# Performance work log

Measured on AMD Instinct MI355X. Metric: run time of the kernel, lower is better.

Reference implementation:

```python
import jax, jax.numpy as jnp
import numpy as np

NUM_AGENTS = 4
ACTOR_DIM = 128
OBS_DIM = 64
ACTION_SIZE = 16
BATCH = 65536


def _linear_params(key, din, dout):
    kw, kb = jax.random.split(key)
    bound = 1.0 / np.sqrt(din)
    W = jax.random.uniform(kw, (din, dout), jnp.float32, -bound, bound)
    b = jax.random.uniform(kb, (dout,), jnp.float32, -bound, bound)
    return W, b


def setup_inputs() -> dict:
    key = jax.random.key(0)
    ks = jax.random.split(key, 8)
    O = jax.random.normal(ks[0], (BATCH, NUM_AGENTS, OBS_DIM), jnp.float32)
    enc_w, enc_b = _linear_params(ks[1], OBS_DIM, ACTOR_DIM)
    fc1_w, fc1_b = _linear_params(ks[2], ACTOR_DIM, ACTOR_DIM)
    fc2_w, fc2_b = _linear_params(ks[3], ACTOR_DIM, ACTOR_DIM)
    fc3_w, fc3_b = _linear_params(ks[4], ACTOR_DIM, ACTOR_DIM)
    cl4_w, cl4_b = _linear_params(ks[5], 2 * ACTOR_DIM, ACTOR_DIM)
    dec_w, dec_b = _linear_params(ks[6], NUM_AGENTS * ACTOR_DIM, ACTION_SIZE)
    return {
        "O": O,
        "enc_w": enc_w, "enc_b": enc_b,
        "fc1_w": fc1_w, "fc1_b": fc1_b,
        "fc2_w": fc2_w, "fc2_b": fc2_b,
        "fc3_w": fc3_w, "fc3_b": fc3_b,
        "cl4_w": cl4_w, "cl4_b": cl4_b,
        "dec_w": dec_w, "dec_b": dec_b,
    }


def reference(O, enc_w, enc_b, fc1_w, fc1_b, fc2_w, fc2_b, fc3_w, fc3_b,
              cl4_w, cl4_b, dec_w, dec_b):
    # Encoding: sigmoid(Linear(obs)) -> [B, A, D]
    H0 = jax.nn.sigmoid(O @ enc_w + enc_b)
    H1 = jax.nn.relu(H0 @ fc1_w + fc1_b)
    H2 = jax.nn.relu(H1 @ fc2_w + fc2_b)
    H3 = jax.nn.relu(H2 @ fc3_w + fc3_b)
    # get_commvar: masked mean over OTHER agents, but torch divides by
    # num_agents (self slot is zeroed then included in the mean).
    # Equivalent fused form: C[b,i] = (sum_j H[b,j] - H[b,i]) / num_agents
    C = (jnp.sum(H3, axis=1, keepdims=True) - H3) / NUM_AGENTS
    H_cat = jnp.concatenate([H3, C], axis=-1)          # [B, A, 2D]
    H4 = H_cat @ cl4_w + cl4_b                          # [B, A, D] (no activation)
    H = H4.reshape(-1, NUM_AGENTS * ACTOR_DIM)          # [B, A*D]
    logits = H @ dec_w + dec_b                          # [B, action_size]
    return jax.nn.softmax(logits, axis=-1)
```

## Files before the change

kernel.cpp:

```cpp
#include <hip/hip_runtime.h>
#include <stdint.h>


typedef __attribute__((ext_vector_type(4)))  float f32x4;
typedef __attribute__((ext_vector_type(16))) float f32x16;
typedef __attribute__((ext_vector_type(8)))  _Float16 f16x8;
typedef __attribute__((ext_vector_type(4)))  _Float16 f16x4;

#define WS_HALF 106496
#define SEG_ENC 0
#define SEG_FC1 8192
#define SEG_FC2 24576
#define SEG_FC3 40960
#define SEG_W1  57344
#define SEG_W2  73728
#define SEG_DEC 90112

#define MFMA16(a, b, c) __builtin_amdgcn_mfma_f32_32x32x16_f16((a), (b), (c), 0, 0, 0)

__device__ __forceinline__ unsigned short f16_bits(float f) {
  union { _Float16 h; unsigned short u; } cv;
  cv.h = (_Float16)f;
  return cv.u;
}
__device__ __forceinline__ f32x16 zero16() {
  f32x16 v;
#pragma unroll
  for (int i = 0; i < 16; ++i) v[i] = 0.0f;
  return v;
}
__device__ __forceinline__ int xswz(int row, int g) {
  return row * 128 + ((g ^ (row & 15)) << 3);
}
__device__ __forceinline__ void barrier_lds() {
  asm volatile("s_waitcnt lgkmcnt(0)\n\ts_barrier" ::: "memory");
}

__global__ void prep_weights(const float* __restrict__ enc_w, const float* __restrict__ fc1_w,
                             const float* __restrict__ fc2_w, const float* __restrict__ fc3_w,
                             const float* __restrict__ cl4_w, const float* __restrict__ dec_w,
                             unsigned short* __restrict__ ws) {
  int idx = blockIdx.x * 256 + threadIdx.x;
  if (idx >= WS_HALF) return;
  const float* W; int base, N, nbN, mode;
  if      (idx <  8192) { W = enc_w; base = SEG_ENC; N = 128; nbN = 4; mode = 0; }
  else if (idx < 24576) { W = fc1_w; base = SEG_FC1; N = 128; nbN = 4; mode = 0; }
  else if (idx < 40960) { W = fc2_w; base = SEG_FC2; N = 128; nbN = 4; mode = 0; }
  else if (idx < 57344) { W = fc3_w; base = SEG_FC3; N = 128; nbN = 4; mode = 0; }
  else if (idx < 73728) { W = cl4_w; base = SEG_W1;  N = 128; nbN = 4; mode = 1; }
  else if (idx < 90112) { W = cl4_w; base = SEG_W2;  N = 128; nbN = 4; mode = 2; }
  else                  { W = dec_w; base = SEG_DEC; N = 16;  nbN = 1; mode = 0; }
  int local = idx - base;
  int j    = local & 7;
  int lane = (local >> 3) & 63;
  int frag = local >> 9;
  int nb = frag % nbN;
  int kc = frag / nbN;
  int k = kc * 16 + ((lane >> 5) << 3) + j;
  int n = nb * 32 + (lane & 31);
  float wv;
  if (mode == 0)      wv = (n < N) ? W[k * N + n] : 0.0f;
  else if (mode == 1) wv = W[k * 128 + n] - 0.25f * W[(k + 128) * 128 + n];
  else                wv = 0.25f * W[(k + 128) * 128 + n];
  ws[idx] = f16_bits(wv);
}

template <int KC, int ACT>
__device__ __forceinline__ void layer_std(const short* __restrict__ Xsrc,
                                          short* __restrict__ Xdst,
                                          const unsigned short* __restrict__ wseg,
                                          const float* __restrict__ bias,
                                          int lr, int lh, int w) {
  const int l = lh * 32 + lr;
  const unsigned short* bp = wseg + w * 512 + l * 8;
  f16x8 Bh[KC];
#pragma unroll
  for (int kc = 0; kc < KC; ++kc) Bh[kc] = *(const f16x8*)(bp + kc * 2048);
  f32x4 bv[4];
#pragma unroll
  for (int q = 0; q < 4; ++q)
    bv[q] = *(const f32x4*)&bias[w * 32 + q * 8 + 4 * lh];
  f32x16 acc0 = zero16(), acc1 = zero16();
#pragma unroll
  for (int kc = 0; kc < KC; ++kc) {
    const int g = kc * 2 + lh;
    const int xi0 = xswz(lr, g), xi1 = xswz(lr + 32, g);
    const f16x8 ah0 = *(const f16x8*)&Xsrc[xi0];
    const f16x8 ah1 = *(const f16x8*)&Xsrc[xi1];
    acc0 = MFMA16(Bh[kc], ah0, acc0);
    acc1 = MFMA16(Bh[kc], ah1, acc1);
  }
#pragma unroll
  for (int mb = 0; mb < 2; ++mb) {
    const int row = mb * 32 + lr;
    const int rb = row & 15;
    const f32x16 a = mb ? acc1 : acc0;
#pragma unroll
    for (int q = 0; q < 4; ++q) {
      f16x4 hq;
#pragma unroll
      for (int t = 0; t < 4; ++t) {
        float v = a[q * 4 + t] + bv[q][t];
        if (ACT == 0)      v = __builtin_amdgcn_rcpf(1.0f + __expf(-v));
        else if (ACT == 1) v = fmaxf(v, 0.0f);
        hq[t] = (_Float16)v;
      }
      const int idx = row * 128 + (((w * 4 + q) ^ rb) << 3) + 4 * lh;
      *(f16x4*)&Xdst[idx] = hq;
    }
  }
}

template <int MB>
__device__ __forceinline__ void cl4_band(const short* __restrict__ Xsrc,
                                         short* __restrict__ Xdst,
                                         const unsigned short* __restrict__ ws,
                                         const float* __restrict__ cl4_b,
                                         int lr, int lh, int w) {
  const int l = lh * 32 + lr;
  const unsigned short* b1p = ws + SEG_W1 + w * 512 + l * 8;
  const unsigned short* b2p = ws + SEG_W2 + w * 512 + l * 8;
  f16x8 B1[4], B2[4];
#pragma unroll
  for (int k = 0; k < 4; ++k) {
    B1[k] = *(const f16x8*)(b1p + k * 2048);
    B2[k] = *(const f16x8*)(b2p + k * 2048);
  }
  f32x4 bv[4];
#pragma unroll
  for (int q = 0; q < 4; ++q)
    bv[q] = *(const f32x4*)&cl4_b[w * 32 + q * 8 + 4 * lh];
  f32x16 a1 = zero16(), a2 = zero16();
#pragma unroll
  for (int kc = 0; kc < 8; ++kc) {
    const int cur = kc & 3;
    const int xi = xswz(MB * 32 + lr, kc * 2 + lh);
    const f16x8 ah = *(const f16x8*)&Xsrc[xi];
    a1 = MFMA16(B1[cur], ah, a1);
    a2 = MFMA16(B2[cur], ah, a2);
    if (kc + 4 < 8) {
      B1[cur] = *(const f16x8*)(b1p + (kc + 4) * 2048);
      B2[cur] = *(const f16x8*)(b2p + (kc + 4) * 2048);
    }
  }
  const int row = MB * 32 + lr;
  const int rb = row & 15;
#pragma unroll
  for (int q = 0; q < 4; ++q) {
    f16x4 hq;
#pragma unroll
    for (int t = 0; t < 4; ++t) {
      const int r = q * 4 + t;
      float t2 = a2[r];
      t2 += __shfl_xor(t2, 1);
      t2 += __shfl_xor(t2, 2);
      hq[t] = (_Float16)(a1[r] + t2 + bv[q][t]);
    }
    const int idx = row * 128 + (((w * 4 + q) ^ rb) << 3) + 4 * lh;
    *(f16x4*)&Xdst[idx] = hq;
  }
}

__global__ __launch_bounds__(256, 4)
void commnet_fwd(const float* __restrict__ O,
                 const float* __restrict__ enc_b, const float* __restrict__ fc1_b,
                 const float* __restrict__ fc2_b, const float* __restrict__ fc3_b,
                 const float* __restrict__ cl4_b, const float* __restrict__ dec_b,
                 const unsigned short* __restrict__ ws, float* __restrict__ out) {
  __shared__ __attribute__((aligned(16))) short X0[64 * 128];
  __shared__ __attribute__((aligned(16))) short X1[64 * 128];
  __shared__ __attribute__((aligned(16))) float Pbuf[272];

  const int tid = threadIdx.x;
  const int l = tid & 63, w = tid >> 6;
  const int lr = l & 31, lh = l >> 5;

  Pbuf[tid] = 0.0f;
  if (tid < 16) Pbuf[256 + tid] = 0.0f;

  {
    const f32x4* Og = (const f32x4*)(O + (long)blockIdx.x * 4096);
#pragma unroll
    for (int it = 0; it < 4; ++it) {
      const int i = it * 256 + tid;
      const int row = i >> 4;
      const int c4 = (i & 15) << 2;
      f32x4 v = Og[i];
      f16x4 hv;
#pragma unroll
      for (int j = 0; j < 4; ++j) hv[j] = (_Float16)v[j];
      const int bi = row * 128 + (((c4 >> 3) ^ (row & 15)) << 3) + (c4 & 7);
      *(f16x4*)&X0[bi] = hv;
    }
  }
  barrier_lds();

  layer_std<4, 0>(X0, X1, ws + SEG_ENC, enc_b, lr, lh, w);
  barrier_lds();
  layer_std<8, 1>(X1, X0, ws + SEG_FC1, fc1_b, lr, lh, w);
  barrier_lds();
  layer_std<8, 1>(X0, X1, ws + SEG_FC2, fc2_b, lr, lh, w);
  barrier_lds();
  layer_std<8, 1>(X1, X0, ws + SEG_FC3, fc3_b, lr, lh, w);
  barrier_lds();

  cl4_band<0>(X0, X1, ws, cl4_b, lr, lh, w);
  cl4_band<1>(X0, X1, ws, cl4_b, lr, lh, w);
  barrier_lds();

  {
    const unsigned short* bp = ws + SEG_DEC + (w * 8) * 512 + l * 8;
    f16x8 Bh[8];
#pragma unroll
    for (int kq = 0; kq < 8; ++kq) Bh[kq] = *(const f16x8*)(bp + kq * 512);
    f32x16 dacc = zero16();
#pragma unroll
    for (int kq = 0; kq < 8; ++kq) {
      const int kcg = w * 8 + kq;
      const int k0 = kcg * 16 + lh * 8;
      const int agent = k0 >> 7;
      const int d0 = k0 & 127;
      const int row = (lr & 15) * 4 + agent;
      const int xi = xswz(row, d0 >> 3);
      const f16x8 ah = *(const f16x8*)&X1[xi];
      dacc = MFMA16(Bh[kq], ah, dacc);
    }
    if (lr < 16) {
#pragma unroll
      for (int r = 0; r < 8; ++r) {
        const int action = (r & 3) + 8 * (r >> 2) + 4 * lh;
        atomicAdd(&Pbuf[lr * 17 + action], dacc[r]);
      }
    }
  }
  barrier_lds();

  {
    const int c = tid & 15;
    float v = Pbuf[(tid >> 4) * 17 + c] + dec_b[c];
    float m = v;
#pragma unroll
    for (int mk = 1; mk < 16; mk <<= 1) m = fmaxf(m, __shfl_xor(m, mk, 16));
    const float e = __expf(v - m);
    float s = e;
#pragma unroll
    for (int mk = 1; mk < 16; mk <<= 1) s += __shfl_xor(s, mk, 16);
    out[(long)blockIdx.x * 256 + tid] = e * __builtin_amdgcn_rcpf(s);
  }
}

extern "C" void kernel_launch(void* const* d_in, const int* in_sizes, int n_in,
                              void* d_out, int out_size, void* d_ws, size_t ws_size,
                              hipStream_t stream) {
  (void)n_in; (void)out_size; (void)ws_size;
  const float* O     = (const float*)d_in[0];
  const float* enc_w = (const float*)d_in[1];
  const float* enc_b = (const float*)d_in[2];
  const float* fc1_w = (const float*)d_in[3];
  const float* fc1_b = (const float*)d_in[4];
  const float* fc2_w = (const float*)d_in[5];
  const float* fc2_b = (const float*)d_in[6];
  const float* fc3_w = (const float*)d_in[7];
  const float* fc3_b = (const float*)d_in[8];
  const float* cl4_w = (const float*)d_in[9];
  const float* cl4_b = (const float*)d_in[10];
  const float* dec_w = (const float*)d_in[11];
  const float* dec_b = (const float*)d_in[12];
  unsigned short* wsb = (unsigned short*)d_ws;

  prep_weights<<<(WS_HALF + 255) / 256, 256, 0, stream>>>(enc_w, fc1_w, fc2_w, fc3_w,
                                                          cl4_w, dec_w, wsb);
  const int rows   = in_sizes[0] / 64;
  const int blocks = rows / 64;
  commnet_fwd<<<blocks, 256, 0, stream>>>(O, enc_b, fc1_b, fc2_b, fc3_b, cl4_b,
                                          dec_b, wsb, (float*)d_out);
}
```

Before: 89.35 us.

## Double block tile to 128 rows and prefetch next layer weights during epilogue

Each block now handles 128 rows with 512 threads (two warp rows times four warp columns), so each weight fragment loaded from global is reused across twice as many rows. Next-layer weight fragments are loaded into a ping-pong register set at the end of each layer, overlapping weight fetch with the barrier and the following layer's start. The larger tile doubles LDS use per block and raises register pressure from holding two 16-fragment buffers, which may reduce occupancy. The decoder now uses all 32 MFMA lanes with fewer k-steps per wave.

```diff
diff --git a/kernel.cpp b/kernel.cpp
--- a/kernel.cpp
+++ b/kernel.cpp
@@ -65,34 +65,32 @@
   ws[idx] = f16_bits(wv);
 }
 
-template <int KC, int ACT>
+template <int KC, int ACT, int KCN>
 __device__ __forceinline__ void layer_std(const short* __restrict__ Xsrc,
                                           short* __restrict__ Xdst,
-                                          const unsigned short* __restrict__ wseg,
+                                          const f16x8 (&Bc)[16],
+                                          const unsigned short* nxt,
+                                          f16x8 (&Bn)[16],
                                           const float* __restrict__ bias,
-                                          int lr, int lh, int w) {
-  const int l = lh * 32 + lr;
-  const unsigned short* bp = wseg + w * 512 + l * 8;
-  f16x8 Bh[KC];
-#pragma unroll
-  for (int kc = 0; kc < KC; ++kc) Bh[kc] = *(const f16x8*)(bp + kc * 2048);
+                                          int lr, int lh, int wr, int wc) {
   f32x4 bv[4];
 #pragma unroll
   for (int q = 0; q < 4; ++q)
-    bv[q] = *(const f32x4*)&bias[w * 32 + q * 8 + 4 * lh];
+    bv[q] = *(const f32x4*)&bias[wc * 32 + q * 8 + 4 * lh];
   f32x16 acc0 = zero16(), acc1 = zero16();
 #pragma unroll
   for (int kc = 0; kc < KC; ++kc) {
     const int g = kc * 2 + lh;
-    const int xi0 = xswz(lr, g), xi1 = xswz(lr + 32, g);
+    const int xi0 = xswz(wr * 64 + lr, g);
+    const int xi1 = xswz(wr * 64 + 32 + lr, g);
     const f16x8 ah0 = *(const f16x8*)&Xsrc[xi0];
     const f16x8 ah1 = *(const f16x8*)&Xsrc[xi1];
-    acc0 = MFMA16(Bh[kc], ah0, acc0);
-    acc1 = MFMA16(Bh[kc], ah1, acc1);
+    acc0 = MFMA16(Bc[kc], ah0, acc0);
+    acc1 = MFMA16(Bc[kc], ah1, acc1);
   }
 #pragma unroll
   for (int mb = 0; mb < 2; ++mb) {
-    const int row = mb * 32 + lr;
+    const int row = wr * 64 + mb * 32 + lr;
     const int rb = row & 15;
     const f32x16 a = mb ? acc1 : acc0;
 #pragma unroll
@@ -105,45 +103,39 @@
         else if (ACT == 1) v = fmaxf(v, 0.0f);
         hq[t] = (_Float16)v;
       }
-      const int idx = row * 128 + (((w * 4 + q) ^ rb) << 3) + 4 * lh;
+      const int idx = row * 128 + (((wc * 4 + q) ^ rb) << 3) + 4 * lh;
       *(f16x4*)&Xdst[idx] = hq;
     }
   }
+#pragma unroll
+  for (int k = 0; k < KCN; ++k)
+    Bn[k] = *(const f16x8*)(nxt + k * 2048);
 }
 
 template <int MB>
 __device__ __forceinline__ void cl4_band(const short* __restrict__ Xsrc,
                                          short* __restrict__ Xdst,
-                                         const unsigned short* __restrict__ ws,
+                                         f16x8 (&B)[16],
+                                         const unsigned short* b2p,
                                          const float* __restrict__ cl4_b,
-                                         int lr, int lh, int w) {
-  const int l = lh * 32 + lr;
-  const unsigned short* b1p = ws + SEG_W1 + w * 512 + l * 8;
-  const unsigned short* b2p = ws + SEG_W2 + w * 512 + l * 8;
-  f16x8 B1[4], B2[4];
-#pragma unroll
-  for (int k = 0; k < 4; ++k) {
-    B1[k] = *(const f16x8*)(b1p + k * 2048);
-    B2[k] = *(const f16x8*)(b2p + k * 2048);
-  }
+                                         int lr, int lh, int wr, int wc) {
   f32x4 bv[4];
 #pragma unroll
   for (int q = 0; q < 4; ++q)
-    bv[q] = *(const f32x4*)&cl4_b[w * 32 + q * 8 + 4 * lh];
+    bv[q] = *(const f32x4*)&cl4_b[wc * 32 + q * 8 + 4 * lh];
   f32x16 a1 = zero16(), a2 = zero16();
 #pragma unroll
   for (int kc = 0; kc < 8; ++kc) {
-    const int cur = kc & 3;
-    const int xi = xswz(MB * 32 + lr, kc * 2 + lh);
+    const int xi = xswz(wr * 64 + MB * 32 + lr, kc * 2 + lh);
     const f16x8 ah = *(const f16x8*)&Xsrc[xi];
-    a1 = MFMA16(B1[cur], ah, a1);
-    a2 = MFMA16(B2[cur], ah, a2);
-    if (kc + 4 < 8) {
-      B1[cur] = *(const f16x8*)(b1p + (kc + 4) * 2048);
-      B2[cur] = *(const f16x8*)(b2p + (kc + 4) * 2048);
-    }
-  }
-  const int row = MB * 32 + lr;
+    a1 = MFMA16(B[kc], ah, a1);
+    a2 = MFMA16(B[8 + (kc & 3)], ah, a2);
+    if (kc < 4) B[8 + kc] = *(const f16x8*)(b2p + (kc + 4) * 2048);
+  }
+#pragma unroll
+  for (int j = 0; j < 4; ++j)
+    B[8 + j] = *(const f16x8*)(b2p + j * 2048);
+  const int row = wr * 64 + MB * 32 + lr;
   const int rb = row & 15;
 #pragma unroll
   for (int q = 0; q < 4; ++q) {
@@ -156,33 +148,42 @@
       t2 += __shfl_xor(t2, 2);
       hq[t] = (_Float16)(a1[r] + t2 + bv[q][t]);
     }
-    const int idx = row * 128 + (((w * 4 + q) ^ rb) << 3) + 4 * lh;
+    const int idx = row * 128 + (((wc * 4 + q) ^ rb) << 3) + 4 * lh;
     *(f16x4*)&Xdst[idx] = hq;
   }
 }
 
-__global__ __launch_bounds__(256, 4)
+__global__ __launch_bounds__(512, 4)
 void commnet_fwd(const float* __restrict__ O,
                  const float* __restrict__ enc_b, const float* __restrict__ fc1_b,
                  const float* __restrict__ fc2_b, const float* __restrict__ fc3_b,
                  const float* __restrict__ cl4_b, const float* __restrict__ dec_b,
                  const unsigned short* __restrict__ ws, float* __restrict__ out) {
-  __shared__ __attribute__((aligned(16))) short X0[64 * 128];
-  __shared__ __attribute__((aligned(16))) short X1[64 * 128];
-  __shared__ __attribute__((aligned(16))) float Pbuf[272];
+  __shared__ __attribute__((aligned(16))) short X0[128 * 128];
+  __shared__ __attribute__((aligned(16))) short X1[128 * 128];
+  __shared__ __attribute__((aligned(16))) float Pbuf[544];
 
   const int tid = threadIdx.x;
   const int l = tid & 63, w = tid >> 6;
   const int lr = l & 31, lh = l >> 5;
+  const int wr = w >> 2, wc = w & 3;
 
   Pbuf[tid] = 0.0f;
-  if (tid < 16) Pbuf[256 + tid] = 0.0f;
-
-  {
-    const f32x4* Og = (const f32x4*)(O + (long)blockIdx.x * 4096);
+  if (tid < 32) Pbuf[512 + tid] = 0.0f;
+
+  f16x8 BA[16], BB[16];
+
+  {
+    const unsigned short* p = ws + SEG_ENC + wc * 512 + l * 8;
+#pragma unroll
+    for (int k = 0; k < 4; ++k) BA[k] = *(const f16x8*)(p + k * 2048);
+  }
+
+  {
+    const f32x4* Og = (const f32x4*)(O + (long)blockIdx.x * 8192);
 #pragma unroll
     for (int it = 0; it < 4; ++it) {
-      const int i = it * 256 + tid;
+      const int i = it * 512 + tid;
       const int row = i >> 4;
       const int c4 = (i & 15) << 2;
       f32x4 v = Og[i];
@@ -195,42 +196,43 @@
   }
   barrier_lds();
 
-  layer_std<4, 0>(X0, X1, ws + SEG_ENC, enc_b, lr, lh, w);
-  barrier_lds();
-  layer_std<8, 1>(X1, X0, ws + SEG_FC1, fc1_b, lr, lh, w);
-  barrier_lds();
-  layer_std<8, 1>(X0, X1, ws + SEG_FC2, fc2_b, lr, lh, w);
-  barrier_lds();
-  layer_std<8, 1>(X1, X0, ws + SEG_FC3, fc3_b, lr, lh, w);
-  barrier_lds();
-
-  cl4_band<0>(X0, X1, ws, cl4_b, lr, lh, w);
-  cl4_band<1>(X0, X1, ws, cl4_b, lr, lh, w);
-  barrier_lds();
-
-  {
-    const unsigned short* bp = ws + SEG_DEC + (w * 8) * 512 + l * 8;
-    f16x8 Bh[8];
-#pragma unroll
-    for (int kq = 0; kq < 8; ++kq) Bh[kq] = *(const f16x8*)(bp + kq * 512);
+  const int base = wc * 512 + l * 8;
+  layer_std<4, 0, 8>(X0, X1, BA, ws + SEG_FC1 + base, BB, enc_b, lr, lh, wr, wc);
+  barrier_lds();
+  layer_std<8, 1, 8>(X1, X0, BB, ws + SEG_FC2 + base, BA, fc1_b, lr, lh, wr, wc);
+  barrier_lds();
+  layer_std<8, 1, 8>(X0, X1, BA, ws + SEG_FC3 + base, BB, fc2_b, lr, lh, wr, wc);
+  barrier_lds();
+  layer_std<8, 1, 12>(X1, X0, BB, ws + SEG_W1 + base, BA, fc3_b, lr, lh, wr, wc);
+  barrier_lds();
+
+  const unsigned short* b2p = ws + SEG_W2 + base;
+  cl4_band<0>(X0, X1, BA, b2p, cl4_b, lr, lh, wr, wc);
+  cl4_band<1>(X0, X1, BA, b2p, cl4_b, lr, lh, wr, wc);
+  {
+    const unsigned short* dp = ws + SEG_DEC + (w * 4) * 512 + l * 8;
+#pragma unroll
+    for (int k = 0; k < 4; ++k) BB[k] = *(const f16x8*)(dp + k * 512);
+  }
+  barrier_lds();
+
+  {
     f32x16 dacc = zero16();
 #pragma unroll
-    for (int kq = 0; kq < 8; ++kq) {
-      const int kcg = w * 8 + kq;
+    for (int kq = 0; kq < 4; ++kq) {
+      const int kcg = w * 4 + kq;
       const int k0 = kcg * 16 + lh * 8;
       const int agent = k0 >> 7;
       const int d0 = k0 & 127;
-      const int row = (lr & 15) * 4 + agent;
+      const int row = lr * 4 + agent;
       const int xi = xswz(row, d0 >> 3);
       const f16x8 ah = *(const f16x8*)&X1[xi];
-      dacc = MFMA16(Bh[kq], ah, dacc);
-    }
-    if (lr < 16) {
-#pragma unroll
-      for (int r = 0; r < 8; ++r) {
-        const int action = (r & 3) + 8 * (r >> 2) + 4 * lh;
-        atomicAdd(&Pbuf[lr * 17 + action], dacc[r]);
-      }
+      dacc = MFMA16(BB[kq], ah, dacc);
+    }
+#pragma unroll
+    for (int r = 0; r < 8; ++r) {
+      const int action = (r & 3) + 8 * (r >> 2) + 4 * lh;
+      atomicAdd(&Pbuf[lr * 17 + action], dacc[r]);
     }
   }
   barrier_lds();
@@ -245,7 +247,7 @@
     float s = e;
 #pragma unroll
     for (int mk = 1; mk < 16; mk <<= 1) s += __shfl_xor(s, mk, 16);
-    out[(long)blockIdx.x * 256 + tid] = e * __builtin_amdgcn_rcpf(s);
+    out[(long)blockIdx.x * 512 + tid] = e * __builtin_amdgcn_rcpf(s);
   }
 }
 
@@ -271,7 +273,7 @@
   prep_weights<<<(WS_HALF + 255) / 256, 256, 0, stream>>>(enc_w, fc1_w, fc2_w, fc3_w,
                                                           cl4_w, dec_w, wsb);
   const int rows   = in_sizes[0] / 64;
-  const int blocks = rows / 64;
-  commnet_fwd<<<blocks, 256, 0, stream>>>(O, enc_b, fc1_b, fc2_b, fc3_b, cl4_b,
+  const int blocks = rows / 128;
+  commnet_fwd<<<blocks, 512, 0, stream>>>(O, enc_b, fc1_b, fc2_b, fc3_b, cl4_b,
                                           dec_b, wsb, (float*)d_out);
 }
```

Result: slower. 117.9 us (+31.9%).
